# Optimization experiments

Measured on AMD Instinct MI355X. Metric: run time of the kernel, lower is better.

Reference implementation:

```python
import jax, jax.numpy as jnp
import numpy as np

N_NODES = 100000
N_EDGES = 3200000
N_GRAPHS = 3200

def setup_inputs() -> dict:
    key = jax.random.key(0)
    ks = jax.random.split(key, 12)
    def glorot(k, shape):
        lim = np.sqrt(6.0 / (shape[0] + shape[1]))
        return jax.random.uniform(k, shape, jnp.float32, -lim, lim)
    x = jax.random.normal(ks[0], (N_NODES, 37), jnp.float32)
    edge_index = jax.random.randint(ks[1], (2, N_EDGES), 0, N_NODES, jnp.int64 if jax.config.jax_enable_x64 else jnp.int32)
    batch = jnp.sort(jax.random.randint(ks[2], (N_NODES,), 0, N_GRAPHS))
    return {
        'x': x,
        'W1': glorot(ks[3], (37, 128)),  'b1': jnp.zeros((128,), jnp.float32),
        'W2': glorot(ks[4], (128, 256)), 'b2': jnp.zeros((256,), jnp.float32),
        'W3': glorot(ks[5], (256, 256)), 'b3': jnp.zeros((256,), jnp.float32),
        'Wp': glorot(ks[6], (256, 256)), 'bp': jnp.zeros((256,), jnp.float32),
        'edge_index': edge_index,
        'batch': batch,
    }

def _gcn_conv(h, W, b, src, dst, dis):
    # PyG GCNConv: h' = D^{-1/2}(A+I)D^{-1/2} (h W) + b, self-loops added
    hW = h @ W
    norm = dis[src] * dis[dst]                      # [E]
    msg = hW[src] * norm[:, None]                   # gather + scale
    agg = jax.ops.segment_sum(msg, dst, num_segments=N_NODES)
    agg = agg + hW * (dis * dis)[:, None]           # self-loop contribution
    return agg + b

def reference(x, W1, b1, W2, b2, W3, b3, Wp, bp, edge_index, batch):
    src, dst = edge_index[0], edge_index[1]
    # degree with self-loops (all edge weights = 1)
    deg = jax.ops.segment_sum(jnp.ones((N_EDGES,), x.dtype), dst, num_segments=N_NODES) + 1.0
    dis = jax.lax.rsqrt(deg)
    h = jax.nn.relu(_gcn_conv(x, W1, b1, src, dst, dis))
    h = jax.nn.relu(_gcn_conv(h, W2, b2, src, dst, dis))
    h = jax.nn.relu(_gcn_conv(h, W3, b3, src, dst, dis))
    # global mean pool over graphs
    sums = jax.ops.segment_sum(h, batch, num_segments=N_GRAPHS)
    cnts = jax.ops.segment_sum(jnp.ones((N_NODES,), x.dtype), batch, num_segments=N_GRAPHS)
    pooled = sums / jnp.maximum(cnts, 1.0)[:, None]
    return pooled @ Wp + bp
```

## Files before the change

kernel.cpp:

```cpp
#include <hip/hip_runtime.h>

#define N_NODES  100000
#define N_EDGES  3200000
#define N_GRAPHS 3200

#define NBLK 200
#define EB   16000
#define BSH  7
#define NB   ((N_NODES + 127) >> BSH)
#define BCAP 5120
#define NT   25
#define TSH  12
#define TP   33

typedef __attribute__((ext_vector_type(8))) short bf16x8;
typedef __attribute__((ext_vector_type(4))) float f32x4;

__device__ __forceinline__ float bf2f(unsigned short u) {
    return __uint_as_float(((unsigned)u) << 16);
}
__device__ __forceinline__ unsigned short f2bf(float f) {
    unsigned u = __float_as_uint(f);
    u += 0x7fffu + ((u >> 16) & 1u);
    return (unsigned short)(u >> 16);
}


__global__ __launch_bounds__(256, 4)
void hist_kernel(const int* __restrict__ dst, int* __restrict__ hist) {
    __shared__ int lh[NB];
    int blk = blockIdx.x, t = threadIdx.x;
    for (int b = t; b < NB; b += 256) lh[b] = 0;
    __syncthreads();
    int e0 = blk * EB;
    for (int i = t; i < EB; i += 256)
        atomicAdd(&lh[dst[e0 + i] >> BSH], 1);
    __syncthreads();
    for (int b = t; b < NB; b += 256) hist[b * NBLK + blk] = lh[b];
}

__global__ void bucket_tot_kernel(const int* __restrict__ hist, int* __restrict__ tot) {
    int b = blockIdx.x, l = threadIdx.x;
    int s = 0;
    for (int k = l; k < NBLK; k += 64) s += hist[b * NBLK + k];
    for (int off = 32; off; off >>= 1) s += __shfl_down(s, off);
    if (l == 0) tot[b] = s;
}

__global__ void bucket_scan_kernel(const int* __restrict__ tot, int* __restrict__ bucketStart) {
    __shared__ int part[256];
    int t = threadIdx.x;
    int chunk = (NB + 255) / 256;
    int lo = t * chunk; if (lo > NB) lo = NB;
    int hi = lo + chunk; if (hi > NB) hi = NB;
    int s = 0;
    for (int i = lo; i < hi; ++i) s += tot[i];
    part[t] = s;
    __syncthreads();
    for (int off = 1; off < 256; off <<= 1) {
        int v = part[t];
        int a = (t >= off) ? part[t - off] : 0;
        __syncthreads();
        part[t] = v + a;
        __syncthreads();
    }
    int run = (t == 0) ? 0 : part[t - 1];
    for (int i = lo; i < hi; ++i) { bucketStart[i] = run; run += tot[i]; }
    if (t == 255) bucketStart[NB] = run;
}

__global__ void bucket_base_kernel(int* __restrict__ hist, const int* __restrict__ bucketStart) {
    int b = blockIdx.x * blockDim.x + threadIdx.x;
    if (b >= NB) return;
    int run = bucketStart[b];
    int* row = hist + b * NBLK;
#pragma unroll 4
    for (int k = 0; k < NBLK; ++k) { int v = row[k]; row[k] = run; run += v; }
}

__global__ __launch_bounds__(256, 4)
void scatter1_kernel(const int* __restrict__ src, const int* __restrict__ dst,
                     const int* __restrict__ base,
                     int* __restrict__ sdst, int* __restrict__ ssrc) {
    __shared__ int lcur[NB];
    int blk = blockIdx.x, t = threadIdx.x;
    for (int b = t; b < NB; b += 256) lcur[b] = base[b * NBLK + blk];
    __syncthreads();
    int e0 = blk * EB;
    for (int i = t; i < EB; i += 256) {
        int d = dst[e0 + i], s = src[e0 + i];
        int pos = atomicAdd(&lcur[d >> BSH], 1);
        sdst[pos] = d;
        ssrc[pos] = s;
    }
}

__global__ __launch_bounds__(256, 1)
void csr2_kernel(const int* __restrict__ sdst, const int* __restrict__ ssrc,
                 const int* __restrict__ bucketStart,
                 int* __restrict__ tileoff, float* __restrict__ dis,
                 int* __restrict__ csr_src) {
    __shared__ int lkey[BCAP];
    __shared__ int lsrc[BCAP];
    __shared__ int lh[128 * TP];
    __shared__ int lc[128 * TP];
    __shared__ int loff[128], ldeg[128];
    int b = blockIdx.x, t = threadIdx.x;
    int n0 = b << BSH;
    int e0 = bucketStart[b], e1 = bucketStart[b + 1];
    int cnt = e1 - e0; if (cnt > BCAP) cnt = BCAP;
    for (int i = t; i < cnt; i += 256) {
        int d = sdst[e0 + i] - n0;
        int s = ssrc[e0 + i];
        lkey[i] = d * TP + (s >> TSH);
        lsrc[i] = s;
    }
    for (int i = t; i < 128 * TP; i += 256) lh[i] = 0;
    __syncthreads();
    for (int i = t; i < cnt; i += 256) atomicAdd(&lh[lkey[i]], 1);
    __syncthreads();
    if (t < 128) {
        int run = 0;
#pragma unroll
        for (int p = 0; p < NT; ++p) { lc[t * TP + p] = run; run += lh[t * TP + p]; }
        ldeg[t] = run;
        loff[t] = run;
    }
    __syncthreads();
    for (int off = 1; off < 128; off <<= 1) {
        int v = 0;
        if (t < 128) { v = loff[t]; if (t >= off) v += loff[t - off]; }
        __syncthreads();
        if (t < 128) loff[t] = v;
        __syncthreads();
    }
    if (t < 128) {
        int excl = loff[t] - ldeg[t];
        int n = n0 + t;
        if (n < N_NODES) {
#pragma unroll
            for (int p = 0; p < NT; ++p) {
                int v = lc[t * TP + p] + excl;
                lc[t * TP + p] = v;
                tileoff[(size_t)n * 26 + p] = e0 + v;
            }
            tileoff[(size_t)n * 26 + NT] = e0 + excl + ldeg[t];
            dis[n] = rsqrtf((float)ldeg[t] + 1.0f);
        } else {
#pragma unroll
            for (int p = 0; p < NT; ++p) lc[t * TP + p] += excl;
        }
    }
    __syncthreads();
    for (int i = t; i < cnt; i += 256) {
        int pos = atomicAdd(&lc[lkey[i]], 1);
        csr_src[e0 + pos] = lsrc[i];
    }
}

template<int K, int N>
__global__ void pack_w_kernel(const float* __restrict__ W, int Krows,
                              unsigned short* __restrict__ hi,
                              unsigned short* __restrict__ lo) {
    constexpr int KS = K / 32;
    int idx = blockIdx.x * blockDim.x + threadIdx.x;
    if (idx >= (N / 16) * KS * 64) return;
    int l = idx & 63;
    int s = (idx >> 6) % KS;
    int t = idx / (64 * KS);
    int k0 = s * 32 + (l >> 4) * 8;
    int n  = t * 16 + (l & 15);
    size_t base = (size_t)idx * 8;
#pragma unroll
    for (int j = 0; j < 8; ++j) {
        int k = k0 + j;
        float w = (k < Krows) ? W[(size_t)k * N + n] : 0.0f;
        unsigned short h = f2bf(w);
        float rem = w - bf2f(h);
        hi[base + j] = h;
        lo[base + j] = f2bf(rem);
    }
}

__global__ __launch_bounds__(256, 4)
void cast_x_kernel(const float* __restrict__ x, const float* __restrict__ dis,
                   unsigned short* __restrict__ xb) {
    int idx = blockIdx.x * blockDim.x + threadIdx.x;
    if (idx >= N_NODES * 64) return;
    int n = idx >> 6, c = idx & 63;
    xb[idx] = (c < 37) ? f2bf(x[(size_t)n * 37 + c] * dis[n]) : (unsigned short)0;
}

template<int F>
__device__ __forceinline__ void agg_range(const unsigned short* __restrict__ tab,
                                          const int* __restrict__ csr_src,
                                          int j, int hi, int lane, float* acc) {
    for (; j + 16 <= hi; j += 16) {
        int sidx[16];
#pragma unroll
        for (int u = 0; u < 16; ++u) sidx[u] = csr_src[j + u];
        if (F == 64) {
            unsigned short v[16];
#pragma unroll
            for (int u = 0; u < 16; ++u) v[u] = tab[(size_t)sidx[u] * 64 + lane];
#pragma unroll
            for (int u = 0; u < 16; ++u) acc[0] += bf2f(v[u]);
        } else if (F == 128) {
            ushort2 v[16];
#pragma unroll
            for (int u = 0; u < 16; ++u)
                v[u] = ((const ushort2*)(tab + (size_t)sidx[u] * F))[lane];
#pragma unroll
            for (int u = 0; u < 16; ++u) { acc[0] += bf2f(v[u].x); acc[1] += bf2f(v[u].y); }
        } else {
            ushort4 v[16];
#pragma unroll
            for (int u = 0; u < 16; ++u)
                v[u] = ((const ushort4*)(tab + (size_t)sidx[u] * F))[lane];
#pragma unroll
            for (int u = 0; u < 16; ++u) {
                acc[0] += bf2f(v[u].x); acc[1] += bf2f(v[u].y);
                acc[2] += bf2f(v[u].z); acc[3] += bf2f(v[u].w);
            }
        }
    }
    for (; j + 4 <= hi; j += 4) {
        int sidx[4];
#pragma unroll
        for (int u = 0; u < 4; ++u) sidx[u] = csr_src[j + u];
        if (F == 64) {
            unsigned short v[4];
#pragma unroll
            for (int u = 0; u < 4; ++u) v[u] = tab[(size_t)sidx[u] * 64 + lane];
#pragma unroll
            for (int u = 0; u < 4; ++u) acc[0] += bf2f(v[u]);
        } else if (F == 128) {
            ushort2 v[4];
#pragma unroll
            for (int u = 0; u < 4; ++u)
                v[u] = ((const ushort2*)(tab + (size_t)sidx[u] * F))[lane];
#pragma unroll
            for (int u = 0; u < 4; ++u) { acc[0] += bf2f(v[u].x); acc[1] += bf2f(v[u].y); }
        } else {
            ushort4 v[4];
#pragma unroll
            for (int u = 0; u < 4; ++u)
                v[u] = ((const ushort4*)(tab + (size_t)sidx[u] * F))[lane];
#pragma unroll
            for (int u = 0; u < 4; ++u) {
                acc[0] += bf2f(v[u].x); acc[1] += bf2f(v[u].y);
                acc[2] += bf2f(v[u].z); acc[3] += bf2f(v[u].w);
            }
        }
    }
    for (; j < hi; ++j) {
        int s = csr_src[j];
        if (F == 64) {
            acc[0] += bf2f(tab[(size_t)s * 64 + lane]);
        } else if (F == 128) {
            ushort2 u = ((const ushort2*)(tab + (size_t)s * F))[lane];
            acc[0] += bf2f(u.x); acc[1] += bf2f(u.y);
        } else {
            ushort4 u = ((const ushort4*)(tab + (size_t)s * F))[lane];
            acc[0] += bf2f(u.x); acc[1] += bf2f(u.y); acc[2] += bf2f(u.z); acc[3] += bf2f(u.w);
        }
    }
}

template<int F>
__global__ __launch_bounds__(256, 4)
void agg_bf16_kernel(const unsigned short* __restrict__ tab,
                     const int* __restrict__ csr_src,
                     const int* __restrict__ tileoff,
                     const float* __restrict__ dis,
                     unsigned short* __restrict__ out) {
    int wave = threadIdx.x >> 6;
    int lane = threadIdx.x & 63;
    int n = blockIdx.x * 4 + wave;

    float acc[(F + 63) / 64];
    if (F == 64) {
        acc[0] = bf2f(tab[(size_t)n * 64 + lane]);
    } else if (F == 128) {
        ushort2 u = ((const ushort2*)(tab + (size_t)n * F))[lane];
        acc[0] = bf2f(u.x); acc[1] = bf2f(u.y);
    } else {
        ushort4 u = ((const ushort4*)(tab + (size_t)n * F))[lane];
        acc[0] = bf2f(u.x); acc[1] = bf2f(u.y); acc[2] = bf2f(u.z); acc[3] = bf2f(u.w);
    }

    int lo = tileoff[(size_t)n * 26 + 0];
    int hi = tileoff[(size_t)n * 26 + NT];
    int deg = hi - lo;
    int jsplit = lo + (int)(((long long)deg * blockIdx.x) / gridDim.x);

    agg_range<F>(tab, csr_src, jsplit, hi, lane, acc);
    agg_range<F>(tab, csr_src, lo, jsplit, lane, acc);

    float d = dis[n];
    if (F == 64) {
        out[(size_t)n * 64 + lane] = f2bf(d * acc[0]);
    } else if (F == 128) {
        ushort2 o; o.x = f2bf(d * acc[0]); o.y = f2bf(d * acc[1]);
        ((ushort2*)(out + (size_t)n * F))[lane] = o;
    } else {
        ushort4 o;
        o.x = f2bf(d * acc[0]); o.y = f2bf(d * acc[1]);
        o.z = f2bf(d * acc[2]); o.w = f2bf(d * acc[3]);
        ((ushort4*)(out + (size_t)n * F))[lane] = o;
    }
}

template<int K, int NTW, int N, int MODE>
__global__ __launch_bounds__(256, 4)
void mfma_gemm_kernel(const unsigned short* __restrict__ A,
                      const unsigned short* __restrict__ Bhi,
                      const unsigned short* __restrict__ Blo,
                      const float* __restrict__ bias,
                      const float* __restrict__ dis,
                      unsigned short* __restrict__ outv) {
    constexpr int KS = K / 32;
    int l   = threadIdx.x & 63;
    int wid = threadIdx.x >> 6;
    int n0  = wid * (NTW * 16);
    int m0  = blockIdx.x * 32;

    f32x4 acc0[NTW], acc1[NTW];
#pragma unroll
    for (int tn = 0; tn < NTW; ++tn) { acc0[tn] = (f32x4){0,0,0,0}; acc1[tn] = (f32x4){0,0,0,0}; }

    const unsigned short* a0 = A + (size_t)(m0 + (l & 15)) * K + (l >> 4) * 8;
    const unsigned short* a1 = a0 + (size_t)16 * K;

#pragma unroll
    for (int s = 0; s < KS; ++s) {
        bf16x8 af0 = *(const bf16x8*)(a0 + s * 32);
        bf16x8 af1 = *(const bf16x8*)(a1 + s * 32);
#pragma unroll
        for (int tn = 0; tn < NTW; ++tn) {
            int t = (n0 >> 4) + tn;
            size_t boff = ((size_t)(t * KS + s) * 64 + l) * 8;
            bf16x8 bh = *(const bf16x8*)(Bhi + boff);
            bf16x8 bl = *(const bf16x8*)(Blo + boff);
            acc0[tn] = __builtin_amdgcn_mfma_f32_16x16x32_bf16(af0, bh, acc0[tn], 0, 0, 0);
            acc0[tn] = __builtin_amdgcn_mfma_f32_16x16x32_bf16(af0, bl, acc0[tn], 0, 0, 0);
            acc1[tn] = __builtin_amdgcn_mfma_f32_16x16x32_bf16(af1, bh, acc1[tn], 0, 0, 0);
            acc1[tn] = __builtin_amdgcn_mfma_f32_16x16x32_bf16(af1, bl, acc1[tn], 0, 0, 0);
        }
    }

    int rowg = (l >> 4) * 4;
#pragma unroll
    for (int tn = 0; tn < NTW; ++tn) {
        int n = n0 + tn * 16 + (l & 15);
        float b = bias[n];
#pragma unroll
        for (int r = 0; r < 4; ++r) {
#pragma unroll
            for (int half = 0; half < 2; ++half) {
                int m = m0 + half * 16 + rowg + r;
                float v = fmaxf((half ? acc1[tn][r] : acc0[tn][r]) + b, 0.0f);
                if (MODE == 1) outv[(size_t)m * N + n] = f2bf(v * dis[m]);
                else           outv[(size_t)m * N + n] = f2bf(v);
            }
        }
    }
}

__device__ __forceinline__ int lower_bound_dev(const int* __restrict__ a, int n, int key) {
    int lo = 0, hi = n;
    while (lo < hi) {
        int mid = (lo + hi) >> 1;
        if (a[mid] < key) lo = mid + 1; else hi = mid;
    }
    return lo;
}

__global__ __launch_bounds__(256, 4)
void pool_bf16_kernel(const unsigned short* __restrict__ h, const int* __restrict__ batch,
                      float* __restrict__ pooled) {
    int wave = threadIdx.x >> 6;
    int lane = threadIdx.x & 63;
    int g = blockIdx.x * 4 + wave;
    int lo = lower_bound_dev(batch, N_NODES, g);
    int hi = lower_bound_dev(batch, N_NODES, g + 1);
    float a0 = 0, a1 = 0, a2 = 0, a3 = 0;
    for (int n = lo; n < hi; ++n) {
        ushort4 u = ((const ushort4*)(h + (size_t)n * 256))[lane];
        a0 += bf2f(u.x); a1 += bf2f(u.y); a2 += bf2f(u.z); a3 += bf2f(u.w);
    }
    float inv = 1.0f / fmaxf((float)(hi - lo), 1.0f);
    float4 o = {a0 * inv, a1 * inv, a2 * inv, a3 * inv};
    *(float4*)&pooled[(size_t)g * 256 + lane * 4] = o;
}

__global__ __launch_bounds__(256, 2)
void head_gemm_kernel(const float* __restrict__ H, const float* __restrict__ W,
                      const float* __restrict__ bias, float* __restrict__ out) {
    __shared__ float lds[16 * 256];
    int row0 = blockIdx.x * 16;
    int t = threadIdx.x;
    const float* src = H + (size_t)row0 * 256;
    for (int i = t; i < 16 * 256; i += 256) lds[i] = src[i];
    __syncthreads();
    float acc[16];
#pragma unroll
    for (int r = 0; r < 16; ++r) acc[r] = 0.0f;
#pragma unroll 4
    for (int k = 0; k < 256; ++k) {
        float wv = W[k * 256 + t];
#pragma unroll
        for (int r = 0; r < 16; ++r) acc[r] += lds[r * 256 + k] * wv;
    }
#pragma unroll
    for (int r = 0; r < 16; ++r)
        out[(size_t)(row0 + r) * 256 + t] = acc[r] + bias[t];
}

static inline size_t align_up(size_t x, size_t a) { return (x + a - 1) & ~(a - 1); }

extern "C" void kernel_launch(void* const* d_in, const int* in_sizes, int n_in,
                              void* d_out, int out_size, void* d_ws, size_t ws_size,
                              hipStream_t stream) {
    const float* x  = (const float*)d_in[0];
    const float* W1 = (const float*)d_in[1];
    const float* b1 = (const float*)d_in[2];
    const float* W2 = (const float*)d_in[3];
    const float* b2 = (const float*)d_in[4];
    const float* W3 = (const float*)d_in[5];
    const float* b3 = (const float*)d_in[6];
    const float* Wp = (const float*)d_in[7];
    const float* bp = (const float*)d_in[8];
    const int*   ei = (const int*)d_in[9];
    const int*   batch = (const int*)d_in[10];
    float* out = (float*)d_out;

    const int* e_src = ei;
    const int* e_dst = ei + N_EDGES;

    char* p = (char*)d_ws;
    size_t off = 0;
    auto take = [&](size_t bytes) {
        void* r = p + off;
        off = align_up(off + bytes, 256);
        return r;
    };
    int*   hist        = (int*)  take(sizeof(int) * NB * NBLK);
    int*   tot         = (int*)  take(sizeof(int) * NB);
    int*   bucketStart = (int*)  take(sizeof(int) * (NB + 1));
    int*   tileoff     = (int*)  take(sizeof(int) * (size_t)N_NODES * 26);
    int*   csr_src     = (int*)  take(sizeof(int) * N_EDGES);
    float* dis         = (float*)take(sizeof(float) * N_NODES);
    float* pooled      = (float*)take(sizeof(float) * N_GRAPHS * 256);
    unsigned short* whi1 = (unsigned short*)take(sizeof(unsigned short) * 64 * 128);
    unsigned short* wlo1 = (unsigned short*)take(sizeof(unsigned short) * 64 * 128);
    unsigned short* whi2 = (unsigned short*)take(sizeof(unsigned short) * 128 * 256);
    unsigned short* wlo2 = (unsigned short*)take(sizeof(unsigned short) * 128 * 256);
    unsigned short* whi3 = (unsigned short*)take(sizeof(unsigned short) * 256 * 256);
    unsigned short* wlo3 = (unsigned short*)take(sizeof(unsigned short) * 256 * 256);
    unsigned short* bufX = (unsigned short*)take(sizeof(unsigned short) * (size_t)N_NODES * 256);
    unsigned short* bufY = (unsigned short*)take(sizeof(unsigned short) * (size_t)N_NODES * 256);
    unsigned short* h3   = (unsigned short*)take(sizeof(unsigned short) * (size_t)N_NODES * 256);

    int* sdst = (int*)h3;
    int* ssrc = sdst + N_EDGES;

    unsigned short* xb     = bufY;
    unsigned short* pbuf1  = bufY + (size_t)N_NODES * 64;
    unsigned short* table2 = bufX;
    unsigned short* pbuf2  = bufX + (size_t)N_NODES * 128;
    unsigned short* table3 = bufY;
    unsigned short* pbuf3  = bufX;

    hist_kernel<<<NBLK, 256, 0, stream>>>(e_dst, hist);
    bucket_tot_kernel<<<NB, 64, 0, stream>>>(hist, tot);
    bucket_scan_kernel<<<1, 256, 0, stream>>>(tot, bucketStart);
    bucket_base_kernel<<<(NB + 255) / 256, 256, 0, stream>>>(hist, bucketStart);
    scatter1_kernel<<<NBLK, 256, 0, stream>>>(e_src, e_dst, hist, sdst, ssrc);
    csr2_kernel<<<NB, 256, 0, stream>>>(sdst, ssrc, bucketStart, tileoff, dis, csr_src);

    pack_w_kernel<64, 128><<<((128 / 16) * 2 * 64 + 255) / 256, 256, 0, stream>>>(W1, 37, whi1, wlo1);
    pack_w_kernel<128, 256><<<((256 / 16) * 4 * 64 + 255) / 256, 256, 0, stream>>>(W2, 128, whi2, wlo2);
    pack_w_kernel<256, 256><<<((256 / 16) * 8 * 64 + 255) / 256, 256, 0, stream>>>(W3, 256, whi3, wlo3);

    cast_x_kernel<<<(N_NODES * 64 + 255) / 256, 256, 0, stream>>>(x, dis, xb);
    agg_bf16_kernel<64><<<N_NODES / 4, 256, 0, stream>>>(xb, csr_src, tileoff, dis, pbuf1);
    mfma_gemm_kernel<64, 2, 128, 1><<<N_NODES / 32, 256, 0, stream>>>(pbuf1, whi1, wlo1, b1, dis, table2);

    agg_bf16_kernel<128><<<N_NODES / 4, 256, 0, stream>>>(table2, csr_src, tileoff, dis, pbuf2);
    mfma_gemm_kernel<128, 4, 256, 1><<<N_NODES / 32, 256, 0, stream>>>(pbuf2, whi2, wlo2, b2, dis, table3);

    agg_bf16_kernel<256><<<N_NODES / 4, 256, 0, stream>>>(table3, csr_src, tileoff, dis, pbuf3);
    mfma_gemm_kernel<256, 4, 256, 2><<<N_NODES / 32, 256, 0, stream>>>(pbuf3, whi3, wlo3, b3, nullptr, h3);

    pool_bf16_kernel<<<N_GRAPHS / 4, 256, 0, stream>>>(h3, batch, pooled);
    head_gemm_kernel<<<N_GRAPHS / 16, 256, 0, stream>>>(pooled, Wp, bp, out);
}
```

Baseline: 739.9 us.

## Fuse neighbor aggregation into MFMA GEMM via swizzled LDS tile and simplify CSR

Merges each layer's gather-aggregation kernel with the following MFMA GEMM. Each block aggregates 32 nodes into an XOR-swizzled LDS tile, then runs the GEMM from LDS, so the intermediate aggregated buffer never goes through global memory. The CSR build drops the per-node source-tile sub-sorting and stores plain offsets, which removes the large tileoff array. In exchange, gathers lose source-locality ordering and the rotated split-start trick, and each block now serializes 8 node aggregations per wave before its GEMM phase.

```diff
diff --git a/kernel.cpp b/kernel.cpp
--- a/kernel.cpp
+++ b/kernel.cpp
@@ -9,9 +9,6 @@
 #define BSH  7
 #define NB   ((N_NODES + 127) >> BSH)
 #define BCAP 5120
-#define NT   25
-#define TSH  12
-#define TP   33
 
 typedef __attribute__((ext_vector_type(8))) short bf16x8;
 typedef __attribute__((ext_vector_type(4))) float f32x4;
@@ -98,34 +95,24 @@
 __global__ __launch_bounds__(256, 1)
 void csr2_kernel(const int* __restrict__ sdst, const int* __restrict__ ssrc,
                  const int* __restrict__ bucketStart,
-                 int* __restrict__ tileoff, float* __restrict__ dis,
+                 int* __restrict__ offsets, float* __restrict__ dis,
                  int* __restrict__ csr_src) {
-    __shared__ int lkey[BCAP];
+    __shared__ int ldst[BCAP];
     __shared__ int lsrc[BCAP];
-    __shared__ int lh[128 * TP];
-    __shared__ int lc[128 * TP];
-    __shared__ int loff[128], ldeg[128];
+    __shared__ int lhist[128], loff[128], lcur[128];
     int b = blockIdx.x, t = threadIdx.x;
     int n0 = b << BSH;
     int e0 = bucketStart[b], e1 = bucketStart[b + 1];
     int cnt = e1 - e0; if (cnt > BCAP) cnt = BCAP;
     for (int i = t; i < cnt; i += 256) {
-        int d = sdst[e0 + i] - n0;
-        int s = ssrc[e0 + i];
-        lkey[i] = d * TP + (s >> TSH);
-        lsrc[i] = s;
-    }
-    for (int i = t; i < 128 * TP; i += 256) lh[i] = 0;
-    __syncthreads();
-    for (int i = t; i < cnt; i += 256) atomicAdd(&lh[lkey[i]], 1);
-    __syncthreads();
-    if (t < 128) {
-        int run = 0;
-#pragma unroll
-        for (int p = 0; p < NT; ++p) { lc[t * TP + p] = run; run += lh[t * TP + p]; }
-        ldeg[t] = run;
-        loff[t] = run;
-    }
+        ldst[i] = sdst[e0 + i] - n0;
+        lsrc[i] = ssrc[e0 + i];
+    }
+    if (t < 128) lhist[t] = 0;
+    __syncthreads();
+    for (int i = t; i < cnt; i += 256) atomicAdd(&lhist[ldst[i]], 1);
+    __syncthreads();
+    if (t < 128) loff[t] = lhist[t];
     __syncthreads();
     for (int off = 1; off < 128; off <<= 1) {
         int v = 0;
@@ -135,25 +122,18 @@
         __syncthreads();
     }
     if (t < 128) {
-        int excl = loff[t] - ldeg[t];
+        int excl = loff[t] - lhist[t];
+        lcur[t] = excl;
         int n = n0 + t;
         if (n < N_NODES) {
-#pragma unroll
-            for (int p = 0; p < NT; ++p) {
-                int v = lc[t * TP + p] + excl;
-                lc[t * TP + p] = v;
-                tileoff[(size_t)n * 26 + p] = e0 + v;
-            }
-            tileoff[(size_t)n * 26 + NT] = e0 + excl + ldeg[t];
-            dis[n] = rsqrtf((float)ldeg[t] + 1.0f);
-        } else {
-#pragma unroll
-            for (int p = 0; p < NT; ++p) lc[t * TP + p] += excl;
-        }
-    }
+            offsets[n] = e0 + excl;
+            dis[n] = rsqrtf((float)lhist[t] + 1.0f);
+        }
+    }
+    if (b == 0 && t == 0) offsets[N_NODES] = N_EDGES;
     __syncthreads();
     for (int i = t; i < cnt; i += 256) {
-        int pos = atomicAdd(&lc[lkey[i]], 1);
+        int pos = atomicAdd(&lcur[ldst[i]], 1);
         csr_src[e0 + pos] = lsrc[i];
     }
 }
@@ -267,75 +247,65 @@
     }
 }
 
-template<int F>
-__global__ __launch_bounds__(256, 4)
-void agg_bf16_kernel(const unsigned short* __restrict__ tab,
-                     const int* __restrict__ csr_src,
-                     const int* __restrict__ tileoff,
-                     const float* __restrict__ dis,
-                     unsigned short* __restrict__ out) {
-    int wave = threadIdx.x >> 6;
-    int lane = threadIdx.x & 63;
-    int n = blockIdx.x * 4 + wave;
-
-    float acc[(F + 63) / 64];
-    if (F == 64) {
-        acc[0] = bf2f(tab[(size_t)n * 64 + lane]);
-    } else if (F == 128) {
-        ushort2 u = ((const ushort2*)(tab + (size_t)n * F))[lane];
-        acc[0] = bf2f(u.x); acc[1] = bf2f(u.y);
-    } else {
-        ushort4 u = ((const ushort4*)(tab + (size_t)n * F))[lane];
-        acc[0] = bf2f(u.x); acc[1] = bf2f(u.y); acc[2] = bf2f(u.z); acc[3] = bf2f(u.w);
-    }
-
-    int lo = tileoff[(size_t)n * 26 + 0];
-    int hi = tileoff[(size_t)n * 26 + NT];
-    int deg = hi - lo;
-    int jsplit = lo + (int)(((long long)deg * blockIdx.x) / gridDim.x);
-
-    agg_range<F>(tab, csr_src, jsplit, hi, lane, acc);
-    agg_range<F>(tab, csr_src, lo, jsplit, lane, acc);
-
-    float d = dis[n];
-    if (F == 64) {
-        out[(size_t)n * 64 + lane] = f2bf(d * acc[0]);
-    } else if (F == 128) {
-        ushort2 o; o.x = f2bf(d * acc[0]); o.y = f2bf(d * acc[1]);
-        ((ushort2*)(out + (size_t)n * F))[lane] = o;
-    } else {
-        ushort4 o;
-        o.x = f2bf(d * acc[0]); o.y = f2bf(d * acc[1]);
-        o.z = f2bf(d * acc[2]); o.w = f2bf(d * acc[3]);
-        ((ushort4*)(out + (size_t)n * F))[lane] = o;
-    }
-}
-
 template<int K, int NTW, int N, int MODE>
 __global__ __launch_bounds__(256, 4)
-void mfma_gemm_kernel(const unsigned short* __restrict__ A,
-                      const unsigned short* __restrict__ Bhi,
-                      const unsigned short* __restrict__ Blo,
-                      const float* __restrict__ bias,
-                      const float* __restrict__ dis,
-                      unsigned short* __restrict__ outv) {
+void fused_agg_gemm(const unsigned short* __restrict__ tab,
+                    const int* __restrict__ csr_src,
+                    const int* __restrict__ offsets,
+                    const float* __restrict__ dis,
+                    const unsigned short* __restrict__ Bhi,
+                    const unsigned short* __restrict__ Blo,
+                    const float* __restrict__ bias,
+                    unsigned short* __restrict__ out) {
     constexpr int KS = K / 32;
-    int l   = threadIdx.x & 63;
-    int wid = threadIdx.x >> 6;
-    int n0  = wid * (NTW * 16);
-    int m0  = blockIdx.x * 32;
-
+    __shared__ unsigned short ldsA[32 * K];
+    char* lb = (char*)ldsA;
+    int l = threadIdx.x & 63;
+    int w = threadIdx.x >> 6;
+    int m0 = blockIdx.x * 32;
+
+    for (int i = 0; i < 8; ++i) {
+        int r = w * 8 + i;
+        int n = m0 + r;
+        float acc[(K + 63) / 64];
+        if (K == 64) {
+            acc[0] = bf2f(tab[(size_t)n * 64 + l]);
+        } else if (K == 128) {
+            ushort2 u = ((const ushort2*)(tab + (size_t)n * K))[l];
+            acc[0] = bf2f(u.x); acc[1] = bf2f(u.y);
+        } else {
+            ushort4 u = ((const ushort4*)(tab + (size_t)n * K))[l];
+            acc[0] = bf2f(u.x); acc[1] = bf2f(u.y); acc[2] = bf2f(u.z); acc[3] = bf2f(u.w);
+        }
+        agg_range<K>(tab, csr_src, offsets[n], offsets[n + 1], l, acc);
+        float d = dis[n];
+        unsigned sw = (unsigned)((r & 7) << 4);
+        if (K == 64) {
+            *(unsigned short*)(lb + ((unsigned)(r * 128 + l * 2) ^ sw)) = f2bf(d * acc[0]);
+        } else if (K == 128) {
+            ushort2 o; o.x = f2bf(d * acc[0]); o.y = f2bf(d * acc[1]);
+            *(ushort2*)(lb + ((unsigned)(r * 256 + l * 4) ^ sw)) = o;
+        } else {
+            ushort4 o;
+            o.x = f2bf(d * acc[0]); o.y = f2bf(d * acc[1]);
+            o.z = f2bf(d * acc[2]); o.w = f2bf(d * acc[3]);
+            *(ushort4*)(lb + ((unsigned)(r * 512 + l * 8) ^ sw)) = o;
+        }
+    }
+    __syncthreads();
+
+    int n0 = w * (NTW * 16);
     f32x4 acc0[NTW], acc1[NTW];
 #pragma unroll
     for (int tn = 0; tn < NTW; ++tn) { acc0[tn] = (f32x4){0,0,0,0}; acc1[tn] = (f32x4){0,0,0,0}; }
 
-    const unsigned short* a0 = A + (size_t)(m0 + (l & 15)) * K + (l >> 4) * 8;
-    const unsigned short* a1 = a0 + (size_t)16 * K;
-
+    int r0 = l & 15, r1 = r0 + 16;
+    unsigned sw0 = (unsigned)((r0 & 7) << 4);
 #pragma unroll
     for (int s = 0; s < KS; ++s) {
-        bf16x8 af0 = *(const bf16x8*)(a0 + s * 32);
-        bf16x8 af1 = *(const bf16x8*)(a1 + s * 32);
+        unsigned kb = (unsigned)(s * 64 + (l >> 4) * 16);
+        bf16x8 af0 = *(const bf16x8*)(lb + ((unsigned)(r0 * K * 2 + kb) ^ sw0));
+        bf16x8 af1 = *(const bf16x8*)(lb + ((unsigned)(r1 * K * 2 + kb) ^ sw0));
 #pragma unroll
         for (int tn = 0; tn < NTW; ++tn) {
             int t = (n0 >> 4) + tn;
@@ -360,8 +330,8 @@
             for (int half = 0; half < 2; ++half) {
                 int m = m0 + half * 16 + rowg + r;
                 float v = fmaxf((half ? acc1[tn][r] : acc0[tn][r]) + b, 0.0f);
-                if (MODE == 1) outv[(size_t)m * N + n] = f2bf(v * dis[m]);
-                else           outv[(size_t)m * N + n] = f2bf(v);
+                if (MODE == 1) out[(size_t)m * N + n] = f2bf(v * dis[m]);
+                else           out[(size_t)m * N + n] = f2bf(v);
             }
         }
     }
@@ -448,7 +418,7 @@
     int*   hist        = (int*)  take(sizeof(int) * NB * NBLK);
     int*   tot         = (int*)  take(sizeof(int) * NB);
     int*   bucketStart = (int*)  take(sizeof(int) * (NB + 1));
-    int*   tileoff     = (int*)  take(sizeof(int) * (size_t)N_NODES * 26);
+    int*   offsets     = (int*)  take(sizeof(int) * (N_NODES + 1));
     int*   csr_src     = (int*)  take(sizeof(int) * N_EDGES);
     float* dis         = (float*)take(sizeof(float) * N_NODES);
     float* pooled      = (float*)take(sizeof(float) * N_GRAPHS * 256);
@@ -466,32 +436,29 @@
     int* ssrc = sdst + N_EDGES;
 
     unsigned short* xb     = bufY;
-    unsigned short* pbuf1  = bufY + (size_t)N_NODES * 64;
     unsigned short* table2 = bufX;
-    unsigned short* pbuf2  = bufX + (size_t)N_NODES * 128;
     unsigned short* table3 = bufY;
-    unsigned short* pbuf3  = bufX;
 
     hist_kernel<<<NBLK, 256, 0, stream>>>(e_dst, hist);
     bucket_tot_kernel<<<NB, 64, 0, stream>>>(hist, tot);
     bucket_scan_kernel<<<1, 256, 0, stream>>>(tot, bucketStart);
     bucket_base_kernel<<<(NB + 255) / 256, 256, 0, stream>>>(hist, bucketStart);
     scatter1_kernel<<<NBLK, 256, 0, stream>>>(e_src, e_dst, hist, sdst, ssrc);
-    csr2_kernel<<<NB, 256, 0, stream>>>(sdst, ssrc, bucketStart, tileoff, dis, csr_src);
+    csr2_kernel<<<NB, 256, 0, stream>>>(sdst, ssrc, bucketStart, offsets, dis, csr_src);
 
     pack_w_kernel<64, 128><<<((128 / 16) * 2 * 64 + 255) / 256, 256, 0, stream>>>(W1, 37, whi1, wlo1);
     pack_w_kernel<128, 256><<<((256 / 16) * 4 * 64 + 255) / 256, 256, 0, stream>>>(W2, 128, whi2, wlo2);
     pack_w_kernel<256, 256><<<((256 / 16) * 8 * 64 + 255) / 256, 256, 0, stream>>>(W3, 256, whi3, wlo3);
 
     cast_x_kernel<<<(N_NODES * 64 + 255) / 256, 256, 0, stream>>>(x, dis, xb);
-    agg_bf16_kernel<64><<<N_NODES / 4, 256, 0, stream>>>(xb, csr_src, tileoff, dis, pbuf1);
-    mfma_gemm_kernel<64, 2, 128, 1><<<N_NODES / 32, 256, 0, stream>>>(pbuf1, whi1, wlo1, b1, dis, table2);
-
-    agg_bf16_kernel<128><<<N_NODES / 4, 256, 0, stream>>>(table2, csr_src, tileoff, dis, pbuf2);
-    mfma_gemm_kernel<128, 4, 256, 1><<<N_NODES / 32, 256, 0, stream>>>(pbuf2, whi2, wlo2, b2, dis, table3);
-
-    agg_bf16_kernel<256><<<N_NODES / 4, 256, 0, stream>>>(table3, csr_src, tileoff, dis, pbuf3);
-    mfma_gemm_kernel<256, 4, 256, 2><<<N_NODES / 32, 256, 0, stream>>>(pbuf3, whi3, wlo3, b3, nullptr, h3);
+    fused_agg_gemm<64, 2, 128, 1><<<N_NODES / 32, 256, 0, stream>>>(
+        xb, csr_src, offsets, dis, whi1, wlo1, b1, table2);
+
+    fused_agg_gemm<128, 4, 256, 1><<<N_NODES / 32, 256, 0, stream>>>(
+        table2, csr_src, offsets, dis, whi2, wlo2, b2, table3);
+
+    fused_agg_gemm<256, 4, 256, 2><<<N_NODES / 32, 256, 0, stream>>>(
+        table3, csr_src, offsets, dis, whi3, wlo3, b3, h3);
 
     pool_bf16_kernel<<<N_GRAPHS / 4, 256, 0, stream>>>(h3, batch, pooled);
     head_gemm_kernel<<<N_GRAPHS / 16, 256, 0, stream>>>(pooled, Wp, bp, out);
```

After: 661.8 us. 10.5% less time.
